# Kernel optimization log

Measured on AMD Instinct MI355X. Metric: run time of the kernel, lower is better.

Reference implementation:

```python
import jax, jax.numpy as jnp
import numpy as np

B, S, H, NH = 2, 2048, 1024, 4
DH = H // NH
EPS_BACKEND = 1e-6
EPS_LN = 1e-6


def setup_inputs() -> dict:
    key = jax.random.key(0)
    kq, kk, kv, kib = jax.random.split(key, 4)
    q = jax.random.normal(kq, (B, S, H), dtype=jnp.float32)
    k = jax.random.normal(kk, (B, S, H), dtype=jnp.float32)
    v = jax.random.normal(kv, (B, S, H), dtype=jnp.float32)
    # gate projections: kernels are zero-initialized in the module
    igate_kernel = jnp.zeros((3 * H, NH), dtype=jnp.float32)
    igate_bias = 0.1 * jax.random.normal(kib, (NH,), dtype=jnp.float32)
    fgate_kernel = jnp.zeros((3 * H, NH), dtype=jnp.float32)
    fgate_bias = jnp.linspace(3.0, 6.0, NH, dtype=jnp.float32)
    outnorm_scale = jnp.ones((H,), dtype=jnp.float32)
    return {"q": q, "k": k, "v": v,
            "igate_kernel": igate_kernel, "igate_bias": igate_bias,
            "fgate_kernel": fgate_kernel, "fgate_bias": fgate_bias,
            "outnorm_scale": outnorm_scale}


def _mlstm_parallel_stabilized(q, k, v, igate_preact, fgate_preact):
    # q,k,v: (B,NH,S,DH); igate_preact,fgate_preact: (B,NH,S,1)
    b, nh, s, dh = q.shape
    log_fg = jax.nn.log_sigmoid(fgate_preact)                       # (B,NH,S,1)
    # cumulative log forget gates, prepended with 0
    cs = jnp.concatenate(
        [jnp.zeros((b, nh, 1), q.dtype), jnp.cumsum(log_fg[..., 0], axis=2)],
        axis=2)                                                      # (B,NH,S+1)
    fg_matrix = cs[:, :, :, None] - cs[:, :, None, :]                # (B,NH,S+1,S+1)
    fg_matrix = fg_matrix[:, :, 1:, 1:]                              # (B,NH,S,S)
    causal = jnp.tril(jnp.ones((s, s), dtype=bool))
    log_fg_matrix = jnp.where(causal, fg_matrix, -jnp.inf)
    log_D = log_fg_matrix + jnp.swapaxes(igate_preact, -2, -1)       # (B,NH,S,S)
    max_log_D = jnp.max(log_D, axis=-1, keepdims=True)               # row-wise stabilizer
    D = jnp.exp(log_D - max_log_D)
    qk = jnp.einsum('bhsd,bhtd->bhst', q, k) / jnp.sqrt(jnp.asarray(dh, q.dtype))
    C = qk * D
    normalizer = jnp.maximum(jnp.abs(jnp.sum(C, axis=-1, keepdims=True)),
                             jnp.exp(-max_log_D))
    C_norm = C / (normalizer + EPS_BACKEND)
    return jnp.einsum('bhst,bhtd->bhsd', C_norm, v)                  # (B,NH,S,DH)


def _multihead_layernorm(x, scale):
    # x: (B,NH,S,DH); per-head LayerNorm over DH (group-norm style), no bias
    mean = jnp.mean(x, axis=-1, keepdims=True)
    var = jnp.var(x, axis=-1, keepdims=True)
    xn = (x - mean) * jax.lax.rsqrt(var + EPS_LN)
    return xn * scale.reshape(NH, 1, DH)


def reference(q, k, v, igate_kernel, igate_bias, fgate_kernel, fgate_bias, outnorm_scale):
    b, s, h = q.shape
    gate_in = jnp.concatenate([q, k, v], axis=-1)                    # (B,S,3H)
    ig = gate_in @ igate_kernel + igate_bias                          # (B,S,NH)
    fg = gate_in @ fgate_kernel + fgate_bias                          # (B,S,NH)
    ig = jnp.transpose(ig, (0, 2, 1))[..., None]                      # (B,NH,S,1)
    fg = jnp.transpose(fg, (0, 2, 1))[..., None]
    qh = jnp.transpose(q.reshape(b, s, NH, DH), (0, 2, 1, 3))         # (B,NH,S,DH)
    kh = jnp.transpose(k.reshape(b, s, NH, DH), (0, 2, 1, 3))
    vh = jnp.transpose(v.reshape(b, s, NH, DH), (0, 2, 1, 3))
    hs = _mlstm_parallel_stabilized(qh, kh, vh, ig, fg)               # (B,NH,S,DH)
    hn = _multihead_layernorm(hs, outnorm_scale)
    return jnp.transpose(hn, (0, 2, 1, 3)).reshape(b, s, h)           # (B,S,H)
```

## Files before the change

### kernel.cpp

```cpp
#include <hip/hip_runtime.h>
#include <hip/hip_bf16.h>
#include <math.h>

#define B_  2
#define S_  2048
#define H_  1024
#define NH_ 4
#define DH_ 256

typedef __attribute__((ext_vector_type(8))) short short8;
typedef __attribute__((ext_vector_type(4))) short short4v;
typedef __attribute__((ext_vector_type(4))) float f32x4;

#define KTILE_BYTES 16384
#define VTILE_BYTES 18432

static __device__ __forceinline__ short f2bf(float x) {
  __hip_bfloat16 h = __float2bfloat16(x);
  union { __hip_bfloat16 h; short s; } u;
  u.h = h;
  return u.s;
}

static __device__ __forceinline__ short8 pack8(const float4& a, const float4& b) {
  short8 t;
  t[0] = f2bf(a.x); t[1] = f2bf(a.y); t[2] = f2bf(a.z); t[3] = f2bf(a.w);
  t[4] = f2bf(b.x); t[5] = f2bf(b.y); t[6] = f2bf(b.z); t[7] = f2bf(b.w);
  return t;
}

static __device__ __forceinline__ void gload16(const void* g, void* l) {
  __builtin_amdgcn_global_load_lds(
      (const __attribute__((address_space(1))) unsigned int*)g,
      (__attribute__((address_space(3))) unsigned int*)l, 16, 0, 0);
}
static __device__ __forceinline__ void gload4(const void* g, void* l) {
  __builtin_amdgcn_global_load_lds(
      (const __attribute__((address_space(1))) unsigned int*)g,
      (__attribute__((address_space(3))) unsigned int*)l, 4, 0, 0);
}

__global__ __launch_bounds__(256) void gates_kernel(
    const float* __restrict__ q, const float* __restrict__ k,
    const float* __restrict__ v,
    const float* __restrict__ igk, const float* __restrict__ igb,
    const float* __restrict__ fgk, const float* __restrict__ fgb,
    float* __restrict__ ig_pre, float* __restrict__ lsf) {
  int bs = blockIdx.x;
  int b = bs / S_, s = bs % S_;
  const float* qrow = q + ((size_t)b * S_ + s) * H_;
  const float* krow = k + ((size_t)b * S_ + s) * H_;
  const float* vrow = v + ((size_t)b * S_ + s) * H_;

  int h0 = threadIdx.x * 4;
  float4 q4 = *reinterpret_cast<const float4*>(qrow + h0);
  float4 k4 = *reinterpret_cast<const float4*>(krow + h0);
  float4 v4 = *reinterpret_cast<const float4*>(vrow + h0);
  float qv[4] = {q4.x, q4.y, q4.z, q4.w};
  float kv[4] = {k4.x, k4.y, k4.z, k4.w};
  float vv[4] = {v4.x, v4.y, v4.z, v4.w};

  const float4* igk4 = reinterpret_cast<const float4*>(igk);
  const float4* fgk4 = reinterpret_cast<const float4*>(fgk);

  float accI[NH_] = {0.f, 0.f, 0.f, 0.f};
  float accF[NH_] = {0.f, 0.f, 0.f, 0.f};
#pragma unroll
  for (int e = 0; e < 4; ++e) {
    int h = h0 + e;
    float4 wiq = igk4[h], wik = igk4[H_ + h], wiv = igk4[2 * H_ + h];
    float4 wfq = fgk4[h], wfk = fgk4[H_ + h], wfv = fgk4[2 * H_ + h];
    accI[0] += qv[e] * wiq.x + kv[e] * wik.x + vv[e] * wiv.x;
    accI[1] += qv[e] * wiq.y + kv[e] * wik.y + vv[e] * wiv.y;
    accI[2] += qv[e] * wiq.z + kv[e] * wik.z + vv[e] * wiv.z;
    accI[3] += qv[e] * wiq.w + kv[e] * wik.w + vv[e] * wiv.w;
    accF[0] += qv[e] * wfq.x + kv[e] * wfk.x + vv[e] * wfv.x;
    accF[1] += qv[e] * wfq.y + kv[e] * wfk.y + vv[e] * wfv.y;
    accF[2] += qv[e] * wfq.z + kv[e] * wfk.z + vv[e] * wfv.z;
    accF[3] += qv[e] * wfq.w + kv[e] * wfk.w + vv[e] * wfv.w;
  }
#pragma unroll
  for (int n = 0; n < NH_; ++n) {
    for (int m = 1; m < 64; m <<= 1) {
      accI[n] += __shfl_xor(accI[n], m);
      accF[n] += __shfl_xor(accF[n], m);
    }
  }
  __shared__ float red[4][8];
  int wave = threadIdx.x >> 6;
  int lane = threadIdx.x & 63;
  if (lane == 0) {
#pragma unroll
    for (int n = 0; n < NH_; ++n) {
      red[wave][n] = accI[n];
      red[wave][4 + n] = accF[n];
    }
  }
  __syncthreads();
  if (threadIdx.x < 8) {
    int t = threadIdx.x;
    float sum = red[0][t] + red[1][t] + red[2][t] + red[3][t];
    if (t < 4) {
      int n = t;
      ig_pre[((size_t)(b * NH_ + n)) * S_ + s] = sum + igb[n];
    } else {
      int n = t - 4;
      float x = sum + fgb[n];
      float ls = (x >= 0.f) ? -log1pf(expf(-x)) : (x - log1pf(expf(x)));
      lsf[((size_t)(b * NH_ + n)) * S_ + s] = ls;
    }
  }
}

__global__ __launch_bounds__(64) void scan_kernel(
    const float* __restrict__ ig_pre, const float* __restrict__ lsf,
    float* __restrict__ a_out, float* __restrict__ M_out,
    float* __restrict__ fl_out) {
  int hd = blockIdx.x;
  int lane = threadIdx.x;
  const float* ig = ig_pre + (size_t)hd * S_;
  const float* ls = lsf + (size_t)hd * S_;
  float xs[32], ys[32];
#pragma unroll
  for (int c = 0; c < 32; ++c) xs[c] = ls[c * 64 + lane];
#pragma unroll
  for (int c = 0; c < 32; ++c) ys[c] = ig[c * 64 + lane];

  float carry = 0.f;
  float mcarry = -INFINITY;
#pragma unroll
  for (int c = 0; c < 32; ++c) {
    int s = c * 64 + lane;
    float x = xs[c];
    for (int off = 1; off < 64; off <<= 1) {
      float t = __shfl_up(x, off);
      if (lane >= off) x += t;
    }
    float csum = carry + x;
    float a = ys[c] - csum;
    float y = a;
    for (int off = 1; off < 64; off <<= 1) {
      float t = __shfl_up(y, off);
      if (lane >= off) y = fmaxf(y, t);
    }
    float M = fmaxf(mcarry, y);
    a_out[(size_t)hd * S_ + s] = a;
    M_out[(size_t)hd * S_ + s] = M;
    fl_out[(size_t)hd * S_ + s] = expf(-(csum + M));
    carry = __shfl(csum, 63);
    mcarry = __shfl(M, 63);
  }
}

__global__ __launch_bounds__(256) void pack_kv(
    const float* __restrict__ k, const float* __restrict__ v,
    char* __restrict__ kpack, char* __restrict__ vpack) {
  const int bidx = blockIdx.x;
  const int hd = bidx & 7, jt = bidx >> 3;
  const int b = hd >> 2, nh = hd & 3;
  const float* kgb = k + ((size_t)b * S_ + jt * 32) * H_ + nh * DH_;
  const float* vgb = v + ((size_t)b * S_ + jt * 32) * H_ + nh * DH_;
  char* kp = kpack + ((size_t)(hd * 64 + jt)) * KTILE_BYTES;
  char* vp = vpack + ((size_t)(hd * 64 + jt)) * VTILE_BYTES;
  const int tid = threadIdx.x;

  {
    int j = tid >> 3, sck = tid & 7;
    const float* row = kgb + (size_t)j * H_ + sck * 32;
    short8* out8 = reinterpret_cast<short8*>(kp) + j * 32;
#pragma unroll
    for (int u = 0; u < 4; ++u) {
      float4 a0 = *reinterpret_cast<const float4*>(row + 8 * u);
      float4 a1 = *reinterpret_cast<const float4*>(row + 8 * u + 4);
      out8[(4 * sck + u) ^ (j & 7)] = pack8(a0, a1);
    }
  }
  {
    int d = tid;
    int jsw = ((d >> 4) & 3) << 3;
    short4v* dst = reinterpret_cast<short4v*>(vp + (size_t)d * 72);
#pragma unroll
    for (int c = 0; c < 8; ++c) {
      short4v t;
#pragma unroll
      for (int e = 0; e < 4; ++e)
        t[e] = f2bf(vgb[(size_t)((4 * c + e) ^ jsw) * H_ + d]);
      dst[c] = t;
    }
    short4v z = {0, 0, 0, 0};
    dst[8] = z;
  }
}

#define KOFF0 0
#define KOFF1 16384
#define VOFF0 32768
#define VOFF1 51200
#define SMEM_BYTES 69632
#define VSTR 36

__global__ __launch_bounds__(256, 2) void mlstm_mfma(
    const float* __restrict__ q,
    const float* __restrict__ a_arr, const float* __restrict__ M_arr,
    const char* __restrict__ kpack, const char* __restrict__ vpack,
    float* __restrict__ outacc, float* __restrict__ po1,
    float* __restrict__ po2, float* __restrict__ po3,
    float* __restrict__ rs0, float* __restrict__ rs1,
    float* __restrict__ rs2, float* __restrict__ rs3) {
  __shared__ __align__(16) char smem[SMEM_BYTES];

  const int bid = blockIdx.x;
  const int half = bid >> 8;
  const int idx = bid & 255;
  const int hd = idx & 7;
  const int u = idx >> 3;
  const int rt = half ? (u & 15) : (15 - (u & 15));
  const int p = half ? (2 + (u >> 4)) : (u >> 4);
  const int ntiles = rt + 1;

  const int b = hd >> 2, nh = hd & 3;
  const int i0 = rt * 128;

  const int tid = threadIdx.x;
  const int wave = tid >> 6;
  const int l = tid & 63;
  const int g = l >> 4;
  const int c16 = l & 15;
  const int iw0 = i0 + wave * 16;
  const int iw1 = i0 + 64 + wave * 16;

  const char* ktiles = kpack + (size_t)hd * 64 * KTILE_BYTES;
  const char* vtiles = vpack + (size_t)hd * 64 * VTILE_BYTES;

  short8 qf0[8], qf1[8];
  {
    const float* qp0 = q + ((size_t)b * S_ + (iw0 + c16)) * H_ + nh * DH_;
    const float* qp1 = q + ((size_t)b * S_ + (iw1 + c16)) * H_ + nh * DH_;
#pragma unroll
    for (int c = 0; c < 8; ++c) {
      int d0 = c * 32 + g * 8;
      qf0[c] = pack8(*reinterpret_cast<const float4*>(qp0 + d0),
                     *reinterpret_cast<const float4*>(qp0 + d0 + 4));
      qf1[c] = pack8(*reinterpret_cast<const float4*>(qp1 + d0),
                     *reinterpret_cast<const float4*>(qp1 + d0 + 4));
    }
  }
  const float Mrs0 = M_arr[(size_t)hd * S_ + iw0 + c16];
  const float Mrs1 = M_arr[(size_t)hd * S_ + iw1 + c16];
  const int i_row0 = iw0 + c16;
  const int i_row1 = iw1 + c16;

  f32x4 oa0[16], oa1[16];
#pragma unroll
  for (int d = 0; d < 16; ++d) {
    oa0[d] = (f32x4){0.f, 0.f, 0.f, 0.f};
    oa1[d] = (f32x4){0.f, 0.f, 0.f, 0.f};
  }
  float rss0 = 0.f, rss1 = 0.f;

  const float* agb = a_arr + (size_t)hd * S_;

  auto stage = [&](int jt, int buf) {
    const char* kt = ktiles + (size_t)jt * KTILE_BYTES + wave * 4096;
    char* kl = smem + (buf ? KOFF1 : KOFF0) + wave * 4096;
#pragma unroll
    for (int uu = 0; uu < 4; ++uu)
      gload16(kt + uu * 1024 + l * 16, kl + uu * 1024);
    const char* vt = vtiles + (size_t)jt * VTILE_BYTES + wave * 4608;
    char* vl = smem + (buf ? VOFF1 : VOFF0) + wave * 4608;
#pragma unroll
    for (int uu = 0; uu < 4; ++uu)
      gload16(vt + uu * 1024 + l * 16, vl + uu * 1024);
#pragma unroll
    for (int uu = 0; uu < 2; ++uu)
      gload4(vt + 4096 + uu * 256 + l * 4, vl + 4096 + uu * 256);
  };

  stage(p, 0);
  __syncthreads();

  for (int n = 0; n < ntiles; ++n) {
    const int jt = p + 4 * n;
    const int cur = n & 1;
    if (n + 1 < ntiles) stage(jt + 4, cur ^ 1);

    {
      const int j0 = jt * 32;
      const short8* kb8 =
          reinterpret_cast<const short8*>(smem + (cur ? KOFF1 : KOFF0));
      const short* vt =
          reinterpret_cast<const short*>(smem + (cur ? VOFF1 : VOFF0));
      f32x4 sa0 = {0.f, 0.f, 0.f, 0.f}, sa1 = {0.f, 0.f, 0.f, 0.f};
      f32x4 sb0 = {0.f, 0.f, 0.f, 0.f}, sb1 = {0.f, 0.f, 0.f, 0.f};
#pragma unroll
      for (int c = 0; c < 8; ++c) {
        int row0 = c16, row1 = 16 + c16;
        int slot = 4 * c + g;
        short8 kf0 = kb8[row0 * 32 + (slot ^ (row0 & 7))];
        short8 kf1 = kb8[row1 * 32 + (slot ^ (row1 & 7))];
        sa0 = __builtin_amdgcn_mfma_f32_16x16x32_bf16(kf0, qf0[c], sa0, 0, 0, 0);
        sa1 = __builtin_amdgcn_mfma_f32_16x16x32_bf16(kf1, qf0[c], sa1, 0, 0, 0);
        sb0 = __builtin_amdgcn_mfma_f32_16x16x32_bf16(kf0, qf1[c], sb0, 0, 0, 0);
        sb1 = __builtin_amdgcn_mfma_f32_16x16x32_bf16(kf1, qf1[c], sb1, 0, 0, 0);
      }
      float4 av0 = *reinterpret_cast<const float4*>(agb + j0 + 4 * g);
      float4 av1 = *reinterpret_cast<const float4*>(agb + j0 + 16 + 4 * g);
      float w00[4], w01[4], w10[4], w11[4];
#pragma unroll
      for (int r = 0; r < 4; ++r) {
        float aa0 = reinterpret_cast<const float*>(&av0)[r];
        float aa1 = reinterpret_cast<const float*>(&av1)[r];
        int j_0 = j0 + 4 * g + r, j_1 = j0 + 16 + 4 * g + r;
        float e00 = __expf(aa0 - Mrs0), e01 = __expf(aa1 - Mrs0);
        float e10 = __expf(aa0 - Mrs1), e11 = __expf(aa1 - Mrs1);
        float t;
        t = sa0[r] * 0.0625f * e00; w00[r] = (j_0 <= i_row0) ? t : 0.f;
        t = sa1[r] * 0.0625f * e01; w01[r] = (j_1 <= i_row0) ? t : 0.f;
        t = sb0[r] * 0.0625f * e10; w10[r] = (j_0 <= i_row1) ? t : 0.f;
        t = sb1[r] * 0.0625f * e11; w11[r] = (j_1 <= i_row1) ? t : 0.f;
        rss0 += w00[r] + w01[r];
        rss1 += w10[r] + w11[r];
      }
      unsigned pA0, pB0, pC0, pD0, pA1, pB1, pC1, pD1;
      asm("v_cvt_pk_bf16_f32 %0, %1, %2" : "=v"(pA0) : "v"(w00[0]), "v"(w00[1]));
      asm("v_cvt_pk_bf16_f32 %0, %1, %2" : "=v"(pB0) : "v"(w00[2]), "v"(w00[3]));
      asm("v_cvt_pk_bf16_f32 %0, %1, %2" : "=v"(pC0) : "v"(w01[0]), "v"(w01[1]));
      asm("v_cvt_pk_bf16_f32 %0, %1, %2" : "=v"(pD0) : "v"(w01[2]), "v"(w01[3]));
      asm("v_cvt_pk_bf16_f32 %0, %1, %2" : "=v"(pA1) : "v"(w10[0]), "v"(w10[1]));
      asm("v_cvt_pk_bf16_f32 %0, %1, %2" : "=v"(pB1) : "v"(w10[2]), "v"(w10[3]));
      asm("v_cvt_pk_bf16_f32 %0, %1, %2" : "=v"(pC1) : "v"(w11[0]), "v"(w11[1]));
      asm("v_cvt_pk_bf16_f32 %0, %1, %2" : "=v"(pD1) : "v"(w11[2]), "v"(w11[3]));
      int src0 = 32 * (g & 1) + c16;
      int src1 = src0 + 16;
      bool lo = (g < 2);
      union { int u[4]; short8 s; } pu0, pu1;
      {
        int a0s = __shfl((int)pA0, src0, 64), b0s = __shfl((int)pB0, src0, 64);
        int c0s = __shfl((int)pC0, src0, 64), d0s = __shfl((int)pD0, src0, 64);
        int a1s = __shfl((int)pA0, src1, 64), b1s = __shfl((int)pB0, src1, 64);
        int c1s = __shfl((int)pC0, src1, 64), d1s = __shfl((int)pD0, src1, 64);
        pu0.u[0] = lo ? a0s : c0s;
        pu0.u[1] = lo ? b0s : d0s;
        pu0.u[2] = lo ? a1s : c1s;
        pu0.u[3] = lo ? b1s : d1s;
      }
      {
        int a0s = __shfl((int)pA1, src0, 64), b0s = __shfl((int)pB1, src0, 64);
        int c0s = __shfl((int)pC1, src0, 64), d0s = __shfl((int)pD1, src0, 64);
        int a1s = __shfl((int)pA1, src1, 64), b1s = __shfl((int)pB1, src1, 64);
        int c1s = __shfl((int)pC1, src1, 64), d1s = __shfl((int)pD1, src1, 64);
        pu1.u[0] = lo ? a0s : c0s;
        pu1.u[1] = lo ? b0s : d0s;
        pu1.u[2] = lo ? a1s : c1s;
        pu1.u[3] = lo ? b1s : d1s;
      }
      short8 pa0 = pu0.s, pa1 = pu1.s;
#pragma unroll
      for (int dq = 0; dq < 16; ++dq) {
        short8 vf = *reinterpret_cast<const short8*>(
            vt + (16 * dq + c16) * VSTR + 8 * (g ^ (dq & 3)));
        oa0[dq] = __builtin_amdgcn_mfma_f32_16x16x32_bf16(pa0, vf, oa0[dq], 0, 0, 0);
        oa1[dq] = __builtin_amdgcn_mfma_f32_16x16x32_bf16(pa1, vf, oa1[dq], 0, 0, 0);
      }
    }
    __syncthreads();
  }

  rss0 += __shfl_xor(rss0, 16);
  rss0 += __shfl_xor(rss0, 32);
  rss1 += __shfl_xor(rss1, 16);
  rss1 += __shfl_xor(rss1, 32);

  float* rsP = (p == 0) ? rs0 : (p == 1) ? rs1 : (p == 2) ? rs2 : rs3;
  if (l < 16) {
    rsP[hd * S_ + iw0 + l] = rss0;
    rsP[hd * S_ + iw1 + l] = rss1;
  }

  if (p == 0) {
#pragma unroll
    for (int dq = 0; dq < 16; ++dq)
#pragma unroll
      for (int r = 0; r < 4; ++r) {
        outacc[((size_t)b * S_ + iw0 + 4 * g + r) * H_ + nh * DH_ +
               dq * 16 + c16] = oa0[dq][r];
        outacc[((size_t)b * S_ + iw1 + 4 * g + r) * H_ + nh * DH_ +
               dq * 16 + c16] = oa1[dq][r];
      }
  } else {
    float* po = (p == 1) ? po1 : (p == 2) ? po2 : po3;
#pragma unroll
    for (int dq = 0; dq < 16; ++dq)
#pragma unroll
      for (int r = 0; r < 4; ++r) {
        po[((size_t)(hd * S_ + iw0 + 4 * g + r)) * DH_ + dq * 16 + c16] =
            oa0[dq][r];
        po[((size_t)(hd * S_ + iw1 + 4 * g + r)) * DH_ + dq * 16 + c16] =
            oa1[dq][r];
      }
  }
}

__global__ __launch_bounds__(256) void combine_kernel(
    const float* __restrict__ po1, const float* __restrict__ po2,
    const float* __restrict__ po3,
    const float* __restrict__ rs0, const float* __restrict__ rs1,
    const float* __restrict__ rs2, const float* __restrict__ rs3,
    const float* __restrict__ fl_arr, const float* __restrict__ scale,
    float* __restrict__ out) {
  int ridx = blockIdx.x * 4 + (threadIdx.x >> 6);
  int lane = threadIdx.x & 63;
  int hd = ridx >> 11, i = ridx & 2047;
  int b = hd >> 2, nh = hd & 3;

  float* op = out + ((size_t)b * S_ + i) * H_ + nh * DH_ + lane * 4;
  float4 a4 = *reinterpret_cast<const float4*>(op);
  size_t poi = ((size_t)(hd * S_ + i)) * DH_ + lane * 4;
  float4 b4 = *reinterpret_cast<const float4*>(po1 + poi);
  float4 c4 = *reinterpret_cast<const float4*>(po2 + poi);
  float4 d4 = *reinterpret_cast<const float4*>(po3 + poi);

  float rsum = rs0[hd * S_ + i] + rs1[hd * S_ + i] + rs2[hd * S_ + i] +
               rs3[hd * S_ + i];
  float o0 = a4.x + b4.x + c4.x + d4.x;
  float o1 = a4.y + b4.y + c4.y + d4.y;
  float o2 = a4.z + b4.z + c4.z + d4.z;
  float o3 = a4.w + b4.w + c4.w + d4.w;

  float fl = fl_arr[(size_t)hd * S_ + i];
  float inv = 1.f / (fmaxf(fabsf(rsum), fl) + 1e-6f);
  o0 *= inv; o1 *= inv; o2 *= inv; o3 *= inv;

  float s1 = o0 + o1 + o2 + o3;
  float s2 = o0 * o0 + o1 * o1 + o2 * o2 + o3 * o3;
#pragma unroll
  for (int m = 1; m < 64; m <<= 1) {
    s1 += __shfl_xor(s1, m);
    s2 += __shfl_xor(s2, m);
  }
  float mean = s1 * (1.f / DH_);
  float var = s2 * (1.f / DH_) - mean * mean;
  float rstd = rsqrtf(var + 1e-6f);

  const float* scp = scale + nh * DH_ + lane * 4;
  float4 res;
  res.x = (o0 - mean) * rstd * scp[0];
  res.y = (o1 - mean) * rstd * scp[1];
  res.z = (o2 - mean) * rstd * scp[2];
  res.w = (o3 - mean) * rstd * scp[3];
  *reinterpret_cast<float4*>(op) = res;
}

extern "C" void kernel_launch(void* const* d_in, const int* in_sizes, int n_in,
                              void* d_out, int out_size, void* d_ws,
                              size_t ws_size, hipStream_t stream) {
  const float* q   = (const float*)d_in[0];
  const float* k   = (const float*)d_in[1];
  const float* v   = (const float*)d_in[2];
  const float* igk = (const float*)d_in[3];
  const float* igb = (const float*)d_in[4];
  const float* fgk = (const float*)d_in[5];
  const float* fgb = (const float*)d_in[6];
  const float* scl = (const float*)d_in[7];
  float* out = (float*)d_out;

  const size_t seq = (size_t)B_ * NH_ * S_;
  const size_t pon = (size_t)8 * 2048 * 256;
  float* ws = (float*)d_ws;
  float* ig_pre = ws;
  float* lsf    = ws + seq;
  float* a_arr  = ws + 2 * seq;
  float* M_arr  = ws + 3 * seq;
  float* fl_arr = ws + 4 * seq;
  float* rs0    = ws + 5 * seq;
  float* rs1    = ws + 6 * seq;
  float* rs2    = ws + 7 * seq;
  float* rs3    = ws + 8 * seq;
  char*  kpack  = (char*)(ws + 9 * seq);
  char*  vpack  = kpack + (size_t)8 * 64 * KTILE_BYTES;
  float* po1    = (float*)(vpack + (size_t)8 * 64 * VTILE_BYTES);
  float* po2    = po1 + pon;
  float* po3    = po2 + pon;

  gates_kernel<<<B_ * S_, 256, 0, stream>>>(q, k, v, igk, igb, fgk, fgb,
                                            ig_pre, lsf);
  scan_kernel<<<B_ * NH_, 64, 0, stream>>>(ig_pre, lsf, a_arr, M_arr, fl_arr);
  pack_kv<<<8 * 64, 256, 0, stream>>>(k, v, kpack, vpack);
  mlstm_mfma<<<512, 256, 0, stream>>>(q, a_arr, M_arr, kpack, vpack,
                                      out, po1, po2, po3,
                                      rs0, rs1, rs2, rs3);
  combine_kernel<<<B_ * NH_ * S_ / 4, 256, 0, stream>>>(
      po1, po2, po3, rs0, rs1, rs2, rs3, fl_arr, scl, out);
}
```

Measured before the change: 162.1 us.

## Load K/V fragments directly from global in MFMA-ready packed layout, dropping LDS staging

The pack kernel now writes K and V tiles in the exact per-lane fragment order the MFMA operands need, so the main kernel reads each short8 fragment straight from global memory. The LDS double-buffering, the async global-to-LDS copies and the per-tile barriers are removed, along with the padded V layout. This removes LDS traffic and synchronisation and frees LDS, which may help occupancy. In exchange, each of the four waves re-reads the same K/V tile through the cache, and there is no explicit prefetch, so global load latency is exposed unless the compiler hoists the loads.

```diff
diff --git a/kernel.cpp b/kernel.cpp
--- a/kernel.cpp
+++ b/kernel.cpp
@@ -9,11 +9,10 @@
 #define DH_ 256
 
 typedef __attribute__((ext_vector_type(8))) short short8;
-typedef __attribute__((ext_vector_type(4))) short short4v;
 typedef __attribute__((ext_vector_type(4))) float f32x4;
 
 #define KTILE_BYTES 16384
-#define VTILE_BYTES 18432
+#define VTILE_BYTES 16384
 
 static __device__ __forceinline__ short f2bf(float x) {
   __hip_bfloat16 h = __float2bfloat16(x);
@@ -27,17 +26,6 @@
   t[0] = f2bf(a.x); t[1] = f2bf(a.y); t[2] = f2bf(a.z); t[3] = f2bf(a.w);
   t[4] = f2bf(b.x); t[5] = f2bf(b.y); t[6] = f2bf(b.z); t[7] = f2bf(b.w);
   return t;
-}
-
-static __device__ __forceinline__ void gload16(const void* g, void* l) {
-  __builtin_amdgcn_global_load_lds(
-      (const __attribute__((address_space(1))) unsigned int*)g,
-      (__attribute__((address_space(3))) unsigned int*)l, 16, 0, 0);
-}
-static __device__ __forceinline__ void gload4(const void* g, void* l) {
-  __builtin_amdgcn_global_load_lds(
-      (const __attribute__((address_space(1))) unsigned int*)g,
-      (__attribute__((address_space(3))) unsigned int*)l, 4, 0, 0);
 }
 
 __global__ __launch_bounds__(256) void gates_kernel(
@@ -165,39 +153,28 @@
   const int tid = threadIdx.x;
 
   {
-    int j = tid >> 3, sck = tid & 7;
-    const float* row = kgb + (size_t)j * H_ + sck * 32;
-    short8* out8 = reinterpret_cast<short8*>(kp) + j * 32;
-#pragma unroll
-    for (int u = 0; u < 4; ++u) {
-      float4 a0 = *reinterpret_cast<const float4*>(row + 8 * u);
-      float4 a1 = *reinterpret_cast<const float4*>(row + 8 * u + 4);
-      out8[(4 * sck + u) ^ (j & 7)] = pack8(a0, a1);
+    int row = tid >> 3, c = tid & 7;
+    const float* src = kgb + (size_t)row * H_ + c * 32;
+#pragma unroll
+    for (int g = 0; g < 4; ++g) {
+      float4 a0 = *reinterpret_cast<const float4*>(src + g * 8);
+      float4 a1 = *reinterpret_cast<const float4*>(src + g * 8 + 4);
+      *reinterpret_cast<short8*>(kp + c * 2048 + g * 512 + row * 16) =
+          pack8(a0, a1);
     }
   }
   {
-    int d = tid;
-    int jsw = ((d >> 4) & 3) << 3;
-    short4v* dst = reinterpret_cast<short4v*>(vp + (size_t)d * 72);
-#pragma unroll
-    for (int c = 0; c < 8; ++c) {
-      short4v t;
-#pragma unroll
-      for (int e = 0; e < 4; ++e)
-        t[e] = f2bf(vgb[(size_t)((4 * c + e) ^ jsw) * H_ + d]);
-      dst[c] = t;
-    }
-    short4v z = {0, 0, 0, 0};
-    dst[8] = z;
-  }
-}
-
-#define KOFF0 0
-#define KOFF1 16384
-#define VOFF0 32768
-#define VOFF1 51200
-#define SMEM_BYTES 69632
-#define VSTR 36
+    int d = tid, dq = d >> 4, cc = d & 15;
+#pragma unroll
+    for (int g = 0; g < 4; ++g) {
+      short8 t;
+#pragma unroll
+      for (int e = 0; e < 8; ++e)
+        t[e] = f2bf(vgb[(size_t)(8 * g + e) * H_ + d]);
+      *reinterpret_cast<short8*>(vp + dq * 1024 + g * 256 + cc * 16) = t;
+    }
+  }
+}
 
 __global__ __launch_bounds__(256, 2) void mlstm_mfma(
     const float* __restrict__ q,
@@ -207,8 +184,6 @@
     float* __restrict__ po2, float* __restrict__ po3,
     float* __restrict__ rs0, float* __restrict__ rs1,
     float* __restrict__ rs2, float* __restrict__ rs3) {
-  __shared__ __align__(16) char smem[SMEM_BYTES];
-
   const int bid = blockIdx.x;
   const int half = bid >> 8;
   const int idx = bid & 255;
@@ -231,6 +206,8 @@
 
   const char* ktiles = kpack + (size_t)hd * 64 * KTILE_BYTES;
   const char* vtiles = vpack + (size_t)hd * 64 * VTILE_BYTES;
+  const int kbase = g * 512 + c16 * 16;
+  const int vbase = g * 256 + c16 * 16;
 
   short8 qf0[8], qf1[8];
   {
@@ -260,110 +237,81 @@
 
   const float* agb = a_arr + (size_t)hd * S_;
 
-  auto stage = [&](int jt, int buf) {
-    const char* kt = ktiles + (size_t)jt * KTILE_BYTES + wave * 4096;
-    char* kl = smem + (buf ? KOFF1 : KOFF0) + wave * 4096;
-#pragma unroll
-    for (int uu = 0; uu < 4; ++uu)
-      gload16(kt + uu * 1024 + l * 16, kl + uu * 1024);
-    const char* vt = vtiles + (size_t)jt * VTILE_BYTES + wave * 4608;
-    char* vl = smem + (buf ? VOFF1 : VOFF0) + wave * 4608;
-#pragma unroll
-    for (int uu = 0; uu < 4; ++uu)
-      gload16(vt + uu * 1024 + l * 16, vl + uu * 1024);
-#pragma unroll
-    for (int uu = 0; uu < 2; ++uu)
-      gload4(vt + 4096 + uu * 256 + l * 4, vl + 4096 + uu * 256);
-  };
-
-  stage(p, 0);
-  __syncthreads();
-
   for (int n = 0; n < ntiles; ++n) {
     const int jt = p + 4 * n;
-    const int cur = n & 1;
-    if (n + 1 < ntiles) stage(jt + 4, cur ^ 1);
-
+    const char* kt = ktiles + (size_t)jt * KTILE_BYTES + kbase;
+    const char* vt = vtiles + (size_t)jt * VTILE_BYTES + vbase;
+    const int j0 = jt * 32;
+
+    f32x4 sa0 = {0.f, 0.f, 0.f, 0.f}, sa1 = {0.f, 0.f, 0.f, 0.f};
+    f32x4 sb0 = {0.f, 0.f, 0.f, 0.f}, sb1 = {0.f, 0.f, 0.f, 0.f};
+#pragma unroll
+    for (int c = 0; c < 8; ++c) {
+      short8 kf0 = *reinterpret_cast<const short8*>(kt + c * 2048);
+      short8 kf1 = *reinterpret_cast<const short8*>(kt + c * 2048 + 256);
+      sa0 = __builtin_amdgcn_mfma_f32_16x16x32_bf16(kf0, qf0[c], sa0, 0, 0, 0);
+      sa1 = __builtin_amdgcn_mfma_f32_16x16x32_bf16(kf1, qf0[c], sa1, 0, 0, 0);
+      sb0 = __builtin_amdgcn_mfma_f32_16x16x32_bf16(kf0, qf1[c], sb0, 0, 0, 0);
+      sb1 = __builtin_amdgcn_mfma_f32_16x16x32_bf16(kf1, qf1[c], sb1, 0, 0, 0);
+    }
+    float4 av0 = *reinterpret_cast<const float4*>(agb + j0 + 4 * g);
+    float4 av1 = *reinterpret_cast<const float4*>(agb + j0 + 16 + 4 * g);
+    float w00[4], w01[4], w10[4], w11[4];
+#pragma unroll
+    for (int r = 0; r < 4; ++r) {
+      float aa0 = reinterpret_cast<const float*>(&av0)[r];
+      float aa1 = reinterpret_cast<const float*>(&av1)[r];
+      int j_0 = j0 + 4 * g + r, j_1 = j0 + 16 + 4 * g + r;
+      float e00 = __expf(aa0 - Mrs0), e01 = __expf(aa1 - Mrs0);
+      float e10 = __expf(aa0 - Mrs1), e11 = __expf(aa1 - Mrs1);
+      float t;
+      t = sa0[r] * 0.0625f * e00; w00[r] = (j_0 <= i_row0) ? t : 0.f;
+      t = sa1[r] * 0.0625f * e01; w01[r] = (j_1 <= i_row0) ? t : 0.f;
+      t = sb0[r] * 0.0625f * e10; w10[r] = (j_0 <= i_row1) ? t : 0.f;
+      t = sb1[r] * 0.0625f * e11; w11[r] = (j_1 <= i_row1) ? t : 0.f;
+      rss0 += w00[r] + w01[r];
+      rss1 += w10[r] + w11[r];
+    }
+    unsigned pA0, pB0, pC0, pD0, pA1, pB1, pC1, pD1;
+    asm("v_cvt_pk_bf16_f32 %0, %1, %2" : "=v"(pA0) : "v"(w00[0]), "v"(w00[1]));
+    asm("v_cvt_pk_bf16_f32 %0, %1, %2" : "=v"(pB0) : "v"(w00[2]), "v"(w00[3]));
+    asm("v_cvt_pk_bf16_f32 %0, %1, %2" : "=v"(pC0) : "v"(w01[0]), "v"(w01[1]));
+    asm("v_cvt_pk_bf16_f32 %0, %1, %2" : "=v"(pD0) : "v"(w01[2]), "v"(w01[3]));
+    asm("v_cvt_pk_bf16_f32 %0, %1, %2" : "=v"(pA1) : "v"(w10[0]), "v"(w10[1]));
+    asm("v_cvt_pk_bf16_f32 %0, %1, %2" : "=v"(pB1) : "v"(w10[2]), "v"(w10[3]));
+    asm("v_cvt_pk_bf16_f32 %0, %1, %2" : "=v"(pC1) : "v"(w11[0]), "v"(w11[1]));
+    asm("v_cvt_pk_bf16_f32 %0, %1, %2" : "=v"(pD1) : "v"(w11[2]), "v"(w11[3]));
+    int src0 = 32 * (g & 1) + c16;
+    int src1 = src0 + 16;
+    bool lo = (g < 2);
+    union { int u[4]; short8 s; } pu0, pu1;
     {
-      const int j0 = jt * 32;
-      const short8* kb8 =
-          reinterpret_cast<const short8*>(smem + (cur ? KOFF1 : KOFF0));
-      const short* vt =
-          reinterpret_cast<const short*>(smem + (cur ? VOFF1 : VOFF0));
-      f32x4 sa0 = {0.f, 0.f, 0.f, 0.f}, sa1 = {0.f, 0.f, 0.f, 0.f};
-      f32x4 sb0 = {0.f, 0.f, 0.f, 0.f}, sb1 = {0.f, 0.f, 0.f, 0.f};
-#pragma unroll
-      for (int c = 0; c < 8; ++c) {
-        int row0 = c16, row1 = 16 + c16;
-        int slot = 4 * c + g;
-        short8 kf0 = kb8[row0 * 32 + (slot ^ (row0 & 7))];
-        short8 kf1 = kb8[row1 * 32 + (slot ^ (row1 & 7))];
-        sa0 = __builtin_amdgcn_mfma_f32_16x16x32_bf16(kf0, qf0[c], sa0, 0, 0, 0);
-        sa1 = __builtin_amdgcn_mfma_f32_16x16x32_bf16(kf1, qf0[c], sa1, 0, 0, 0);
-        sb0 = __builtin_amdgcn_mfma_f32_16x16x32_bf16(kf0, qf1[c], sb0, 0, 0, 0);
-        sb1 = __builtin_amdgcn_mfma_f32_16x16x32_bf16(kf1, qf1[c], sb1, 0, 0, 0);
-      }
-      float4 av0 = *reinterpret_cast<const float4*>(agb + j0 + 4 * g);
-      float4 av1 = *reinterpret_cast<const float4*>(agb + j0 + 16 + 4 * g);
-      float w00[4], w01[4], w10[4], w11[4];
-#pragma unroll
-      for (int r = 0; r < 4; ++r) {
-        float aa0 = reinterpret_cast<const float*>(&av0)[r];
-        float aa1 = reinterpret_cast<const float*>(&av1)[r];
-        int j_0 = j0 + 4 * g + r, j_1 = j0 + 16 + 4 * g + r;
-        float e00 = __expf(aa0 - Mrs0), e01 = __expf(aa1 - Mrs0);
-        float e10 = __expf(aa0 - Mrs1), e11 = __expf(aa1 - Mrs1);
-        float t;
-        t = sa0[r] * 0.0625f * e00; w00[r] = (j_0 <= i_row0) ? t : 0.f;
-        t = sa1[r] * 0.0625f * e01; w01[r] = (j_1 <= i_row0) ? t : 0.f;
-        t = sb0[r] * 0.0625f * e10; w10[r] = (j_0 <= i_row1) ? t : 0.f;
-        t = sb1[r] * 0.0625f * e11; w11[r] = (j_1 <= i_row1) ? t : 0.f;
-        rss0 += w00[r] + w01[r];
-        rss1 += w10[r] + w11[r];
-      }
-      unsigned pA0, pB0, pC0, pD0, pA1, pB1, pC1, pD1;
-      asm("v_cvt_pk_bf16_f32 %0, %1, %2" : "=v"(pA0) : "v"(w00[0]), "v"(w00[1]));
-      asm("v_cvt_pk_bf16_f32 %0, %1, %2" : "=v"(pB0) : "v"(w00[2]), "v"(w00[3]));
-      asm("v_cvt_pk_bf16_f32 %0, %1, %2" : "=v"(pC0) : "v"(w01[0]), "v"(w01[1]));
-      asm("v_cvt_pk_bf16_f32 %0, %1, %2" : "=v"(pD0) : "v"(w01[2]), "v"(w01[3]));
-      asm("v_cvt_pk_bf16_f32 %0, %1, %2" : "=v"(pA1) : "v"(w10[0]), "v"(w10[1]));
-      asm("v_cvt_pk_bf16_f32 %0, %1, %2" : "=v"(pB1) : "v"(w10[2]), "v"(w10[3]));
-      asm("v_cvt_pk_bf16_f32 %0, %1, %2" : "=v"(pC1) : "v"(w11[0]), "v"(w11[1]));
-      asm("v_cvt_pk_bf16_f32 %0, %1, %2" : "=v"(pD1) : "v"(w11[2]), "v"(w11[3]));
-      int src0 = 32 * (g & 1) + c16;
-      int src1 = src0 + 16;
-      bool lo = (g < 2);
-      union { int u[4]; short8 s; } pu0, pu1;
-      {
-        int a0s = __shfl((int)pA0, src0, 64), b0s = __shfl((int)pB0, src0, 64);
-        int c0s = __shfl((int)pC0, src0, 64), d0s = __shfl((int)pD0, src0, 64);
-        int a1s = __shfl((int)pA0, src1, 64), b1s = __shfl((int)pB0, src1, 64);
-        int c1s = __shfl((int)pC0, src1, 64), d1s = __shfl((int)pD0, src1, 64);
-        pu0.u[0] = lo ? a0s : c0s;
-        pu0.u[1] = lo ? b0s : d0s;
-        pu0.u[2] = lo ? a1s : c1s;
-        pu0.u[3] = lo ? b1s : d1s;
-      }
-      {
-        int a0s = __shfl((int)pA1, src0, 64), b0s = __shfl((int)pB1, src0, 64);
-        int c0s = __shfl((int)pC1, src0, 64), d0s = __shfl((int)pD1, src0, 64);
-        int a1s = __shfl((int)pA1, src1, 64), b1s = __shfl((int)pB1, src1, 64);
-        int c1s = __shfl((int)pC1, src1, 64), d1s = __shfl((int)pD1, src1, 64);
-        pu1.u[0] = lo ? a0s : c0s;
-        pu1.u[1] = lo ? b0s : d0s;
-        pu1.u[2] = lo ? a1s : c1s;
-        pu1.u[3] = lo ? b1s : d1s;
-      }
-      short8 pa0 = pu0.s, pa1 = pu1.s;
-#pragma unroll
-      for (int dq = 0; dq < 16; ++dq) {
-        short8 vf = *reinterpret_cast<const short8*>(
-            vt + (16 * dq + c16) * VSTR + 8 * (g ^ (dq & 3)));
-        oa0[dq] = __builtin_amdgcn_mfma_f32_16x16x32_bf16(pa0, vf, oa0[dq], 0, 0, 0);
-        oa1[dq] = __builtin_amdgcn_mfma_f32_16x16x32_bf16(pa1, vf, oa1[dq], 0, 0, 0);
-      }
-    }
-    __syncthreads();
+      int a0s = __shfl((int)pA0, src0, 64), b0s = __shfl((int)pB0, src0, 64);
+      int c0s = __shfl((int)pC0, src0, 64), d0s = __shfl((int)pD0, src0, 64);
+      int a1s = __shfl((int)pA0, src1, 64), b1s = __shfl((int)pB0, src1, 64);
+      int c1s = __shfl((int)pC0, src1, 64), d1s = __shfl((int)pD0, src1, 64);
+      pu0.u[0] = lo ? a0s : c0s;
+      pu0.u[1] = lo ? b0s : d0s;
+      pu0.u[2] = lo ? a1s : c1s;
+      pu0.u[3] = lo ? b1s : d1s;
+    }
+    {
+      int a0s = __shfl((int)pA1, src0, 64), b0s = __shfl((int)pB1, src0, 64);
+      int c0s = __shfl((int)pC1, src0, 64), d0s = __shfl((int)pD1, src0, 64);
+      int a1s = __shfl((int)pA1, src1, 64), b1s = __shfl((int)pB1, src1, 64);
+      int c1s = __shfl((int)pC1, src1, 64), d1s = __shfl((int)pD1, src1, 64);
+      pu1.u[0] = lo ? a0s : c0s;
+      pu1.u[1] = lo ? b0s : d0s;
+      pu1.u[2] = lo ? a1s : c1s;
+      pu1.u[3] = lo ? b1s : d1s;
+    }
+    short8 pa0 = pu0.s, pa1 = pu1.s;
+#pragma unroll
+    for (int dq = 0; dq < 16; ++dq) {
+      short8 vf = *reinterpret_cast<const short8*>(vt + dq * 1024);
+      oa0[dq] = __builtin_amdgcn_mfma_f32_16x16x32_bf16(pa0, vf, oa0[dq], 0, 0, 0);
+      oa1[dq] = __builtin_amdgcn_mfma_f32_16x16x32_bf16(pa1, vf, oa1[dq], 0, 0, 0);
+    }
   }
 
   rss0 += __shfl_xor(rss0, 16);
```

After: 188.8 us. 16.5% more time.

## Store split-K partial outputs as bf16 and merge scan into pack kernel

Applied to the files above, without the earlier changes.

The four split partial output accumulators are now written as bf16 into a separate workspace instead of fp32, including the p==0 partial that previously went straight into the output. The combine kernel reads four bf16 partials and converts them back to float. This halves partial-output traffic. Separately, the scan and K/V pack kernels are merged into one launch, with 8 extra blocks doing the scan, which saves a launch. The cost is lower precision on the unnormalized partial sums before normalization and layernorm.

```diff
diff --git a/kernel.cpp b/kernel.cpp
--- a/kernel.cpp
+++ b/kernel.cpp
@@ -20,6 +20,12 @@
   union { __hip_bfloat16 h; short s; } u;
   u.h = h;
   return u.s;
+}
+
+static __device__ __forceinline__ float bf2f(short s) {
+  union { unsigned u; float f; } t;
+  t.u = ((unsigned)(unsigned short)s) << 16;
+  return t.f;
 }
 
 static __device__ __forceinline__ short8 pack8(const float4& a, const float4& b) {
@@ -112,50 +118,51 @@
   }
 }
 
-__global__ __launch_bounds__(64) void scan_kernel(
+__global__ __launch_bounds__(256) void pack_scan_kernel(
+    const float* __restrict__ k, const float* __restrict__ v,
+    char* __restrict__ kpack, char* __restrict__ vpack,
     const float* __restrict__ ig_pre, const float* __restrict__ lsf,
     float* __restrict__ a_out, float* __restrict__ M_out,
     float* __restrict__ fl_out) {
-  int hd = blockIdx.x;
-  int lane = threadIdx.x;
-  const float* ig = ig_pre + (size_t)hd * S_;
-  const float* ls = lsf + (size_t)hd * S_;
-  float xs[32], ys[32];
-#pragma unroll
-  for (int c = 0; c < 32; ++c) xs[c] = ls[c * 64 + lane];
-#pragma unroll
-  for (int c = 0; c < 32; ++c) ys[c] = ig[c * 64 + lane];
-
-  float carry = 0.f;
-  float mcarry = -INFINITY;
-#pragma unroll
-  for (int c = 0; c < 32; ++c) {
-    int s = c * 64 + lane;
-    float x = xs[c];
-    for (int off = 1; off < 64; off <<= 1) {
-      float t = __shfl_up(x, off);
-      if (lane >= off) x += t;
-    }
-    float csum = carry + x;
-    float a = ys[c] - csum;
-    float y = a;
-    for (int off = 1; off < 64; off <<= 1) {
-      float t = __shfl_up(y, off);
-      if (lane >= off) y = fmaxf(y, t);
-    }
-    float M = fmaxf(mcarry, y);
-    a_out[(size_t)hd * S_ + s] = a;
-    M_out[(size_t)hd * S_ + s] = M;
-    fl_out[(size_t)hd * S_ + s] = expf(-(csum + M));
-    carry = __shfl(csum, 63);
-    mcarry = __shfl(M, 63);
-  }
-}
-
-__global__ __launch_bounds__(256) void pack_kv(
-    const float* __restrict__ k, const float* __restrict__ v,
-    char* __restrict__ kpack, char* __restrict__ vpack) {
   const int bidx = blockIdx.x;
+  if (bidx >= 512) {
+    if (threadIdx.x >= 64) return;
+    int hd = bidx - 512;
+    int lane = threadIdx.x;
+    const float* ig = ig_pre + (size_t)hd * S_;
+    const float* ls = lsf + (size_t)hd * S_;
+    float xs[32], ys[32];
+#pragma unroll
+    for (int c = 0; c < 32; ++c) xs[c] = ls[c * 64 + lane];
+#pragma unroll
+    for (int c = 0; c < 32; ++c) ys[c] = ig[c * 64 + lane];
+    float carry = 0.f;
+    float mcarry = -INFINITY;
+#pragma unroll
+    for (int c = 0; c < 32; ++c) {
+      int s = c * 64 + lane;
+      float x = xs[c];
+      for (int off = 1; off < 64; off <<= 1) {
+        float t = __shfl_up(x, off);
+        if (lane >= off) x += t;
+      }
+      float csum = carry + x;
+      float a = ys[c] - csum;
+      float y = a;
+      for (int off = 1; off < 64; off <<= 1) {
+        float t = __shfl_up(y, off);
+        if (lane >= off) y = fmaxf(y, t);
+      }
+      float M = fmaxf(mcarry, y);
+      a_out[(size_t)hd * S_ + s] = a;
+      M_out[(size_t)hd * S_ + s] = M;
+      fl_out[(size_t)hd * S_ + s] = expf(-(csum + M));
+      carry = __shfl(csum, 63);
+      mcarry = __shfl(M, 63);
+    }
+    return;
+  }
+
   const int hd = bidx & 7, jt = bidx >> 3;
   const int b = hd >> 2, nh = hd & 3;
   const float* kgb = k + ((size_t)b * S_ + jt * 32) * H_ + nh * DH_;
@@ -203,8 +210,8 @@
     const float* __restrict__ q,
     const float* __restrict__ a_arr, const float* __restrict__ M_arr,
     const char* __restrict__ kpack, const char* __restrict__ vpack,
-    float* __restrict__ outacc, float* __restrict__ po1,
-    float* __restrict__ po2, float* __restrict__ po3,
+    short* __restrict__ po0, short* __restrict__ po1,
+    short* __restrict__ po2, short* __restrict__ po3,
     float* __restrict__ rs0, float* __restrict__ rs1,
     float* __restrict__ rs2, float* __restrict__ rs3) {
   __shared__ __align__(16) char smem[SMEM_BYTES];
@@ -377,33 +384,21 @@
     rsP[hd * S_ + iw1 + l] = rss1;
   }
 
-  if (p == 0) {
-#pragma unroll
-    for (int dq = 0; dq < 16; ++dq)
-#pragma unroll
-      for (int r = 0; r < 4; ++r) {
-        outacc[((size_t)b * S_ + iw0 + 4 * g + r) * H_ + nh * DH_ +
-               dq * 16 + c16] = oa0[dq][r];
-        outacc[((size_t)b * S_ + iw1 + 4 * g + r) * H_ + nh * DH_ +
-               dq * 16 + c16] = oa1[dq][r];
-      }
-  } else {
-    float* po = (p == 1) ? po1 : (p == 2) ? po2 : po3;
-#pragma unroll
-    for (int dq = 0; dq < 16; ++dq)
-#pragma unroll
-      for (int r = 0; r < 4; ++r) {
-        po[((size_t)(hd * S_ + iw0 + 4 * g + r)) * DH_ + dq * 16 + c16] =
-            oa0[dq][r];
-        po[((size_t)(hd * S_ + iw1 + 4 * g + r)) * DH_ + dq * 16 + c16] =
-            oa1[dq][r];
-      }
-  }
+  short* po = (p == 0) ? po0 : (p == 1) ? po1 : (p == 2) ? po2 : po3;
+#pragma unroll
+  for (int dq = 0; dq < 16; ++dq)
+#pragma unroll
+    for (int r = 0; r < 4; ++r) {
+      po[((size_t)(hd * S_ + iw0 + 4 * g + r)) * DH_ + dq * 16 + c16] =
+          f2bf(oa0[dq][r]);
+      po[((size_t)(hd * S_ + iw1 + 4 * g + r)) * DH_ + dq * 16 + c16] =
+          f2bf(oa1[dq][r]);
+    }
 }
 
 __global__ __launch_bounds__(256) void combine_kernel(
-    const float* __restrict__ po1, const float* __restrict__ po2,
-    const float* __restrict__ po3,
+    const short* __restrict__ po0, const short* __restrict__ po1,
+    const short* __restrict__ po2, const short* __restrict__ po3,
     const float* __restrict__ rs0, const float* __restrict__ rs1,
     const float* __restrict__ rs2, const float* __restrict__ rs3,
     const float* __restrict__ fl_arr, const float* __restrict__ scale,
@@ -413,19 +408,18 @@
   int hd = ridx >> 11, i = ridx & 2047;
   int b = hd >> 2, nh = hd & 3;
 
-  float* op = out + ((size_t)b * S_ + i) * H_ + nh * DH_ + lane * 4;
-  float4 a4 = *reinterpret_cast<const float4*>(op);
   size_t poi = ((size_t)(hd * S_ + i)) * DH_ + lane * 4;
-  float4 b4 = *reinterpret_cast<const float4*>(po1 + poi);
-  float4 c4 = *reinterpret_cast<const float4*>(po2 + poi);
-  float4 d4 = *reinterpret_cast<const float4*>(po3 + poi);
+  short4v a4 = *reinterpret_cast<const short4v*>(po0 + poi);
+  short4v b4 = *reinterpret_cast<const short4v*>(po1 + poi);
+  short4v c4 = *reinterpret_cast<const short4v*>(po2 + poi);
+  short4v d4 = *reinterpret_cast<const short4v*>(po3 + poi);
 
   float rsum = rs0[hd * S_ + i] + rs1[hd * S_ + i] + rs2[hd * S_ + i] +
                rs3[hd * S_ + i];
-  float o0 = a4.x + b4.x + c4.x + d4.x;
-  float o1 = a4.y + b4.y + c4.y + d4.y;
-  float o2 = a4.z + b4.z + c4.z + d4.z;
-  float o3 = a4.w + b4.w + c4.w + d4.w;
+  float o0 = bf2f(a4[0]) + bf2f(b4[0]) + bf2f(c4[0]) + bf2f(d4[0]);
+  float o1 = bf2f(a4[1]) + bf2f(b4[1]) + bf2f(c4[1]) + bf2f(d4[1]);
+  float o2 = bf2f(a4[2]) + bf2f(b4[2]) + bf2f(c4[2]) + bf2f(d4[2]);
+  float o3 = bf2f(a4[3]) + bf2f(b4[3]) + bf2f(c4[3]) + bf2f(d4[3]);
 
   float fl = fl_arr[(size_t)hd * S_ + i];
   float inv = 1.f / (fmaxf(fabsf(rsum), fl) + 1e-6f);
@@ -448,6 +442,7 @@
   res.y = (o1 - mean) * rstd * scp[1];
   res.z = (o2 - mean) * rstd * scp[2];
   res.w = (o3 - mean) * rstd * scp[3];
+  float* op = out + ((size_t)b * S_ + i) * H_ + nh * DH_ + lane * 4;
   *reinterpret_cast<float4*>(op) = res;
 }
 
@@ -478,17 +473,18 @@
   float* rs3    = ws + 8 * seq;
   char*  kpack  = (char*)(ws + 9 * seq);
   char*  vpack  = kpack + (size_t)8 * 64 * KTILE_BYTES;
-  float* po1    = (float*)(vpack + (size_t)8 * 64 * VTILE_BYTES);
-  float* po2    = po1 + pon;
-  float* po3    = po2 + pon;
+  short* po0    = (short*)(vpack + (size_t)8 * 64 * VTILE_BYTES);
+  short* po1    = po0 + pon;
+  short* po2    = po1 + pon;
+  short* po3    = po2 + pon;
 
   gates_kernel<<<B_ * S_, 256, 0, stream>>>(q, k, v, igk, igb, fgk, fgb,
                                             ig_pre, lsf);
-  scan_kernel<<<B_ * NH_, 64, 0, stream>>>(ig_pre, lsf, a_arr, M_arr, fl_arr);
-  pack_kv<<<8 * 64, 256, 0, stream>>>(k, v, kpack, vpack);
+  pack_scan_kernel<<<520, 256, 0, stream>>>(k, v, kpack, vpack,
+                                            ig_pre, lsf, a_arr, M_arr, fl_arr);
   mlstm_mfma<<<512, 256, 0, stream>>>(q, a_arr, M_arr, kpack, vpack,
-                                      out, po1, po2, po3,
+                                      po0, po1, po2, po3,
                                       rs0, rs1, rs2, rs3);
   combine_kernel<<<B_ * NH_ * S_ / 4, 256, 0, stream>>>(
-      po1, po2, po3, rs0, rs1, rs2, rs3, fl_arr, scl, out);
-}
+      po0, po1, po2, po3, rs0, rs1, rs2, rs3, fl_arr, scl, out);
+}
```

After: 156.1 us. 1.04x faster.
